# Kernel optimization log

Hardware: AMD Instinct MI355X
Metric: run time of the kernel (lower is better)

The kernel has to match this reference:

```python
import jax, jax.numpy as jnp
import numpy as np
from jax import lax

NUM_TAGS = 19
IN_DIM = 202
HID = 100
B, T = 256, 512


def setup_inputs() -> dict:
    key = jax.random.key(0)
    ks = jax.random.split(key, 16)
    u = lambda k, shape, s: jax.random.uniform(k, shape, jnp.float32, -s, s)
    sh = 1.0 / np.sqrt(HID)
    sl = 1.0 / np.sqrt(2 * HID)
    x = jax.random.normal(ks[0], (B, T, IN_DIM), jnp.float32)
    lengths = jax.random.randint(ks[1], (B,), 1, T + 1)
    raw_tags = jax.random.randint(ks[2], (B, T), 0, NUM_TAGS)
    y = jnp.where(jnp.arange(T)[None, :] < lengths[:, None], raw_tags, -1)
    return dict(
        x=x, y=y,
        w_ih_f=u(ks[3], (HID, IN_DIM), sh), w_hh_f=u(ks[4], (HID, HID), sh),
        b_ih_f=u(ks[5], (HID,), sh), b_hh_f=u(ks[6], (HID,), sh),
        w_ih_b=u(ks[7], (HID, IN_DIM), sh), w_hh_b=u(ks[8], (HID, HID), sh),
        b_ih_b=u(ks[9], (HID,), sh), b_hh_b=u(ks[10], (HID,), sh),
        w_lin=u(ks[11], (NUM_TAGS, 2 * HID), sl), b_lin=u(ks[12], (NUM_TAGS,), sl),
        start_trans=u(ks[13], (NUM_TAGS,), 0.1),
        end_trans=u(ks[14], (NUM_TAGS,), 0.1),
        trans=u(ks[15], (NUM_TAGS, NUM_TAGS), 0.1),
    )


def _rnn_dir(x, w_ih, w_hh, b_ih, b_hh, reverse):
    # torch nn.RNN (tanh) scans over axis 0 of x (batch_first=False semantics)
    def step(h, xt):
        h = jnp.tanh(xt @ w_ih.T + b_ih + h @ w_hh.T + b_hh)
        return h, h
    h0 = jnp.zeros((x.shape[1], w_hh.shape[0]), x.dtype)
    _, hs = lax.scan(step, h0, x, reverse=reverse)
    return hs  # (S, N, HID)


def _emissions(x, w_ih_f, w_hh_f, b_ih_f, b_hh_f, w_ih_b, w_hh_b, b_ih_b, b_hh_b, w_lin, b_lin):
    hf = _rnn_dir(x, w_ih_f, w_hh_f, b_ih_f, b_hh_f, False)
    hb = _rnn_dir(x, w_ih_b, w_hh_b, b_ih_b, b_hh_b, True)
    h = jnp.concatenate([hf, hb], axis=-1)  # (B, T, 200)
    return jax.nn.softmax(h @ w_lin.T + b_lin, axis=2)  # (B, T, 19)


def _crf_llh(em, tags, mask, start, end, trans):
    # emissions (B,T,K) batch_first -> transpose to (T,B,*) for the scans
    em_t = jnp.swapaxes(em, 0, 1)
    tg = jnp.where(jnp.swapaxes(mask, 0, 1), jnp.swapaxes(tags, 0, 1), 0)
    mk = jnp.swapaxes(mask, 0, 1)
    mf = mk.astype(em.dtype)
    # numerator: gold path score
    s0 = start[tg[0]] + jnp.take_along_axis(em_t[0], tg[0][:, None], 1)[:, 0]
    def num_step(carry, inp):
        s, prev = carry
        e, t, m, mb = inp
        emit = jnp.take_along_axis(e, t[:, None], 1)[:, 0]
        s = s + (trans[prev, t] + emit) * m
        prev = jnp.where(mb, t, prev)  # track tag at last valid position
        return (s, prev), None
    (num, last), _ = lax.scan(num_step, (s0, tg[0]), (em_t[1:], tg[1:], mf[1:], mk[1:]))
    num = num + end[last]
    # denominator: masked forward algorithm
    def z_step(s, inp):
        e, mb = inp
        nxt = jax.nn.logsumexp(s[:, :, None] + trans[None] + e[:, None, :], axis=1)
        return jnp.where(mb[:, None], nxt, s), None
    z, _ = lax.scan(z_step, start + em_t[0], (em_t[1:], mk[1:]))
    logz = jax.nn.logsumexp(z + end, axis=1)
    return num - logz  # (B,) log-likelihood per sequence


def _viterbi(em, mask, start, end, trans):
    em_t = jnp.swapaxes(em, 0, 1)
    mk = jnp.swapaxes(mask, 0, 1)
    def fstep(s, inp):
        e, mb = inp
        cand = s[:, :, None] + trans[None] + e[:, None, :]  # (B,K,K)
        nxt = jnp.where(mb[:, None], jnp.max(cand, axis=1), s)
        return nxt, jnp.argmax(cand, axis=1)
    score, hist = lax.scan(fstep, start + em_t[0], (em_t[1:], mk[1:]))  # hist (T-1,B,K)
    best_last = jnp.argmax(score + end, axis=1)  # tag at each sequence end
    def bstep(tag, inp):
        h, mb = inp
        prev = jnp.take_along_axis(h, tag[:, None], 1)[:, 0]
        tag = jnp.where(mb, prev, tag)
        return tag, tag
    _, tags_bt = lax.scan(bstep, best_last, (hist, mk[1:]), reverse=True)  # (T-1,B), position order
    tags = jnp.concatenate([tags_bt, best_last[None]], axis=0)  # (T,B)
    tags = jnp.swapaxes(tags, 0, 1)
    return jnp.where(mask, tags, -1)  # pad with -1 like the torch pad_sequence


def reference(x, y, w_ih_f, w_hh_f, b_ih_f, b_hh_f, w_ih_b, w_hh_b, b_ih_b, b_hh_b, w_lin, b_lin, start_trans, end_trans, trans):
    mask = y != -1
    em = _emissions(x, w_ih_f, w_hh_f, b_ih_f, b_hh_f, w_ih_b, w_hh_b, b_ih_b, b_hh_b, w_lin, b_lin)
    loss = -jnp.sum(_crf_llh(em, y, mask, start_trans, end_trans, trans))  # reduction='sum'
    label = _viterbi(em, mask, start_trans, end_trans, trans)
    return loss, label
```

## Files before the change

kernel.cpp:

```cpp
#include <hip/hip_runtime.h>
#include <hip/hip_bf16.h>

#define B_ 256
#define T_ 512
#define IN_ 202
#define HID_ 100
#define K_ 19

typedef __attribute__((ext_vector_type(8))) short short8v;
typedef __attribute__((ext_vector_type(4))) float f32x4;

__device__ __forceinline__ float rl_f(float v, int l) {
  return __int_as_float(__builtin_amdgcn_readlane(__float_as_int(v), l));
}
__device__ __forceinline__ float bcast_f(float v, int l) {
  return __int_as_float(__builtin_amdgcn_ds_bpermute(l * 4, __float_as_int(v)));
}
__device__ __forceinline__ float fast_tanh(float x) {
  float t = __expf(2.f * x);
  float r = __builtin_amdgcn_rcpf(t + 1.f);
  return fmaf(-2.f, r, 1.f);
}

__global__ __launch_bounds__(256, 1) void k_wprep(
    const float* __restrict__ wf, const float* __restrict__ wb,
    unsigned short* __restrict__ w3) {
  int idx = blockIdx.x * 256 + threadIdx.x;
  if (idx >= 224 * 224) return;
  int c = idx / 224, k = idx - (idx / 224) * 224;
  float v = 0.f;
  if (k < IN_) {
    if (c < 100) v = wf[c * IN_ + k];
    else if (c < 200) v = wb[(c - 100) * IN_ + k];
  }
  unsigned u0 = __float_as_uint(v) & 0xffff0000u;
  float r1 = v - __uint_as_float(u0);
  unsigned u1 = __float_as_uint(r1) & 0xffff0000u;
  float r2 = r1 - __uint_as_float(u1);
  w3[idx] = (unsigned short)(u0 >> 16);
  w3[50176 + idx] = (unsigned short)(u1 >> 16);
  w3[100352 + idx] = (unsigned short)(__float_as_uint(r2) >> 16);
}

__global__ __launch_bounds__(256, 2) void k_ih(
    const float* __restrict__ x, const unsigned short* __restrict__ w3,
    const float* __restrict__ bif, const float* __restrict__ bhf,
    const float* __restrict__ bib, const float* __restrict__ bhb,
    float* __restrict__ pre) {
  __shared__ float xs[128 * 36];
  __shared__ float bsum[224];
  int tid = threadIdx.x;
  int wv = tid >> 6, l = tid & 63;
  long row0 = (long)blockIdx.x * 128;
  for (int u = tid; u < 224; u += 256) {
    float bv = 0.f;
    if (u < 100) bv = bif[u] + bhf[u];
    else if (u < 200) bv = bib[u - 100] + bhb[u - 100];
    bsum[u] = bv;
  }
  int lr = l & 15;
  int kq = l >> 4;
  f32x4 acc[2][14];
#pragma unroll
  for (int m = 0; m < 2; m++)
#pragma unroll
    for (int n = 0; n < 14; n++) acc[m][n] = (f32x4){0.f, 0.f, 0.f, 0.f};
  for (int ck = 0; ck < 7; ck++) {
    int k0 = ck * 32;
    __syncthreads();
#pragma unroll
    for (int i = 0; i < 8; i++) {
      int u = tid + i * 256;
      int r = u >> 4, kp = u & 15;
      int gk = k0 + 2 * kp;
      float2 v = make_float2(0.f, 0.f);
      if (gk < IN_) v = *(const float2*)(x + (row0 + r) * IN_ + gk);
      *(float2*)(&xs[r * 36 + 2 * kp]) = v;
    }
    __syncthreads();
    short8v A0[2], A1[2], A2[2];
#pragma unroll
    for (int m = 0; m < 2; m++) {
      const float* ap = &xs[(wv * 32 + m * 16 + lr) * 36 + kq * 8];
      float4 fa = *(const float4*)(ap);
      float4 fb = *(const float4*)(ap + 4);
      float f[8] = {fa.x, fa.y, fa.z, fa.w, fb.x, fb.y, fb.z, fb.w};
#pragma unroll
      for (int j = 0; j < 8; j++) {
        unsigned u0 = __float_as_uint(f[j]) & 0xffff0000u;
        float r1 = f[j] - __uint_as_float(u0);
        unsigned u1 = __float_as_uint(r1) & 0xffff0000u;
        float r2 = r1 - __uint_as_float(u1);
        A0[m][j] = (short)(u0 >> 16);
        A1[m][j] = (short)(u1 >> 16);
        A2[m][j] = (short)(__float_as_uint(r2) >> 16);
      }
    }
#pragma unroll
    for (int n = 0; n < 14; n++) {
      int col = n * 16 + lr;
      const unsigned short* bp = w3 + (long)col * 224 + k0 + kq * 8;
      short8v B0 = *(const short8v*)(bp);
      short8v B1 = *(const short8v*)(bp + 50176);
      short8v B2 = *(const short8v*)(bp + 100352);
#pragma unroll
      for (int m = 0; m < 2; m++) {
        f32x4 c = acc[m][n];
        c = __builtin_amdgcn_mfma_f32_16x16x32_bf16(A0[m], B0, c, 0, 0, 0);
        c = __builtin_amdgcn_mfma_f32_16x16x32_bf16(A0[m], B1, c, 0, 0, 0);
        c = __builtin_amdgcn_mfma_f32_16x16x32_bf16(A1[m], B0, c, 0, 0, 0);
        c = __builtin_amdgcn_mfma_f32_16x16x32_bf16(A0[m], B2, c, 0, 0, 0);
        c = __builtin_amdgcn_mfma_f32_16x16x32_bf16(A2[m], B0, c, 0, 0, 0);
        c = __builtin_amdgcn_mfma_f32_16x16x32_bf16(A1[m], B1, c, 0, 0, 0);
        c = __builtin_amdgcn_mfma_f32_16x16x32_bf16(A1[m], B2, c, 0, 0, 0);
        c = __builtin_amdgcn_mfma_f32_16x16x32_bf16(A2[m], B1, c, 0, 0, 0);
        acc[m][n] = c;
      }
    }
  }
#pragma unroll
  for (int m = 0; m < 2; m++) {
    long rbase = row0 + wv * 32 + m * 16 + kq * 4;
#pragma unroll
    for (int n = 0; n < 13; n++) {
      int col = n * 16 + lr;
      if (col < 200) {
        float bv = bsum[col];
#pragma unroll
        for (int r = 0; r < 4; r++)
          pre[(rbase + r) * 200 + col] = acc[m][n][r] + bv;
      }
    }
  }
}

template <int KO, int KN, bool OW>
__device__ __forceinline__ void rnn8(
    float* __restrict__ p, long step, int row, bool owns, int qidx,
    const float* __restrict__ w, float (*hb)[104], float (*ps)[104]) {
  float wr[KN];
#pragma unroll
  for (int i = 0; i < KN / 4; i++) {
    float4 w4 = *(const float4*)(w + row * HID_ + KO + 4 * i);
    wr[4 * i + 0] = w4.x; wr[4 * i + 1] = w4.y;
    wr[4 * i + 2] = w4.z; wr[4 * i + 3] = w4.w;
  }
  float a = 0.f;
  if (OW) a = p[row];
  for (int s = 0; s < B_; s++) {
    int cur = s & 1;
    float a_next = 0.f;
    if (OW && s < B_ - 1) a_next = p[step + row];
    float ac0 = OW ? a : 0.f, ac1 = 0.f, ac2 = 0.f, ac3 = 0.f;
#pragma unroll
    for (int i = 0; i < KN / 4; i++) {
      float4 h4 = *(const float4*)(&hb[cur][KO + 4 * i]);
      ac0 = fmaf(h4.x, wr[4 * i + 0], ac0);
      ac1 = fmaf(h4.y, wr[4 * i + 1], ac1);
      ac2 = fmaf(h4.z, wr[4 * i + 2], ac2);
      ac3 = fmaf(h4.w, wr[4 * i + 3], ac3);
    }
    float partial = (ac0 + ac1) + (ac2 + ac3);
    if (!OW && owns) ps[qidx][row] = partial;
    __syncthreads();
    if (OW) {
      float tot = partial + ps[0][row] + ps[1][row] + ps[2][row];
      float hnew = fast_tanh(tot);
      if (owns) {
        p[row] = hnew;
        hb[cur ^ 1][row] = hnew;
      }
    }
    __syncthreads();
    p += step;
    a = a_next;
  }
}

__global__ __launch_bounds__(512, 8) void k_rnn(
    float* __restrict__ pre,
    const float* __restrict__ whf, const float* __restrict__ whb) {
  __shared__ __align__(16) float hb[2][104];
  __shared__ __align__(16) float ps[3][104];
  int bid = blockIdx.x;
  int dir = bid >> 9;
  int t = bid & 511;
  const float* w = dir ? whb : whf;
  int tid = threadIdx.x;
  int wv = tid >> 6, lane = tid & 63;
  int grp = wv & 1;
  int kq = wv >> 1;
  int row = grp ? (64 + (lane < 36 ? lane : 35)) : lane;
  bool owns = grp ? (lane < 36) : true;
  long step = dir ? -(long)(T_ * 200) : (long)(T_ * 200);
  float* p = pre + ((long)(dir ? (B_ - 1) : 0) * T_ + t) * 200 + dir * 100;
  if (tid < 104) hb[0][tid] = 0.f;
  __syncthreads();
  if (kq == 0)      rnn8<0, 16, true >(p, step, row, owns, 0, w, hb, ps);
  else if (kq == 1) rnn8<16, 28, false>(p, step, row, owns, 0, w, hb, ps);
  else if (kq == 2) rnn8<44, 28, false>(p, step, row, owns, 1, w, hb, ps);
  else              rnn8<72, 28, false>(p, step, row, owns, 2, w, hb, ps);
}

__global__ __launch_bounds__(256, 4) void k_lin(
    const float* __restrict__ h, const float* __restrict__ wlin,
    const float* __restrict__ blin, float* __restrict__ em) {
  int tid = threadIdx.x;
  long r0 = ((long)blockIdx.x * 256 + tid) * 2;
  const float* h0 = h + r0 * 200;
  float acc0[K_], acc1[K_];
#pragma unroll
  for (int c = 0; c < K_; c++) { float bb = blin[c]; acc0[c] = bb; acc1[c] = bb; }
  for (int kk = 0; kk < 50; kk++) {
    float4 a = *(const float4*)(h0 + 4 * kk);
    float4 b = *(const float4*)(h0 + 200 + 4 * kk);
#pragma unroll
    for (int c = 0; c < K_; c++) {
      float4 wv = *(const float4*)(wlin + c * 200 + 4 * kk);
      acc0[c] += a.x * wv.x + a.y * wv.y + a.z * wv.z + a.w * wv.w;
      acc1[c] += b.x * wv.x + b.y * wv.y + b.z * wv.z + b.w * wv.w;
    }
  }
  float mx0 = acc0[0], mx1 = acc1[0];
#pragma unroll
  for (int c = 1; c < K_; c++) { mx0 = fmaxf(mx0, acc0[c]); mx1 = fmaxf(mx1, acc1[c]); }
  float s0 = 0.f, s1 = 0.f;
#pragma unroll
  for (int c = 0; c < K_; c++) {
    acc0[c] = __expf(acc0[c] - mx0); s0 += acc0[c];
    acc1[c] = __expf(acc1[c] - mx1); s1 += acc1[c];
  }
  float i0 = 1.f / s0, i1 = 1.f / s1;
  float* e0 = em + r0 * K_;
#pragma unroll
  for (int c = 0; c < K_; c++) { e0[c] = acc0[c] * i0; e0[K_ + c] = acc1[c] * i1; }
}

__global__ __launch_bounds__(128, 1) void k_crf(
    const float* __restrict__ em, const int* __restrict__ y,
    const float* __restrict__ st_g, const float* __restrict__ en_g,
    const float* __restrict__ tr_g,
    float* __restrict__ part, int* __restrict__ cnt,
    float* __restrict__ out) {
  __shared__ __align__(16) float es[T_ * K_];
  __shared__ int ys[T_];
  __shared__ float trs[K_ * K_];
  __shared__ float st[K_], en[K_];
  __shared__ unsigned char hl[511 * K_ + 13];
  int b = blockIdx.x;
  int tid = threadIdx.x;
  int wv = tid >> 6, lane = tid & 63;
  const float4* eb4 = (const float4*)(em + (long)b * T_ * K_);
  for (int u = tid; u < T_ * K_ / 4; u += 128) ((float4*)es)[u] = eb4[u];
  for (int u = tid; u < T_; u += 128) ys[u] = y[b * T_ + u];
  for (int u = tid; u < K_ * K_; u += 128) trs[u] = tr_g[u];
  if (tid < K_) { st[tid] = st_g[tid]; en[tid] = en_g[tid]; }
  __syncthreads();
  int lmin = T_;
  for (int u = lane; u < T_; u += 64)
    if (ys[u] == -1 && u < lmin) lmin = u;
#pragma unroll
  for (int off = 32; off; off >>= 1) {
    int o = __shfl_xor(lmin, off, 64);
    lmin = lmin < o ? lmin : o;
  }
  int len = lmin;

  int jj = lane < K_ ? lane : K_ - 1;
  bool act = lane < K_;
  float enr[20];
#pragma unroll
  for (int q = 0; q < 5; q++) {
    float4 e4 = (q < 4) ? *(const float4*)(&en[4 * q])
                        : make_float4(en[16], en[17], en[18], -1e30f);
    enr[4 * q] = e4.x; enr[4 * q + 1] = e4.y; enr[4 * q + 2] = e4.z; enr[4 * q + 3] = e4.w;
  }

  if (wv == 0) {
    float gacc = 0.f;
    for (int t = 1 + lane; t < len; t += 64)
      gacc += trs[ys[t - 1] * K_ + ys[t]] + es[t * K_ + ys[t]];
#pragma unroll
    for (int off = 32; off; off >>= 1) gacc += __shfl_xor(gacc, off, 64);
    int y0 = ys[0], ylast = ys[len - 1];
    float num = st[y0] + es[y0] + gacc + en[ylast];
    float Ecol[K_];
#pragma unroll
    for (int i = 0; i < K_; i++) Ecol[i] = __expf(trs[i * K_ + jj]);
    float P = __expf(st[jj] + es[jj]);
    int kacc = 0;
    float ee = __expf(es[K_ + jj]);
    for (int t = 1; t < len; t++) {
      float pr[K_];
#pragma unroll
      for (int i = 0; i < K_; i++) pr[i] = bcast_f(P, i);
      int tn = (t + 1 < T_) ? t + 1 : T_ - 1;
      float e_next = es[tn * K_ + jj];
      unsigned pb = __float_as_uint(pr[0]);
      int ex = (int)((pb >> 23) & 0xff);
      float scale = __uint_as_float((unsigned)(254 - ex) << 23);
      kacc += ex - 127;
      float a0 = 0.f, a1 = 0.f, a2 = 0.f, a3 = 0.f;
#pragma unroll
      for (int i = 0; i < K_; i++) {
        if ((i & 3) == 0)      a0 = fmaf(pr[i], Ecol[i], a0);
        else if ((i & 3) == 1) a1 = fmaf(pr[i], Ecol[i], a1);
        else if ((i & 3) == 2) a2 = fmaf(pr[i], Ecol[i], a2);
        else                   a3 = fmaf(pr[i], Ecol[i], a3);
      }
      P = ((((a0 + a1) + (a2 + a3)) * ee)) * scale;
      ee = __expf(e_next);
    }
    {
      float pr[K_];
#pragma unroll
      for (int i = 0; i < K_; i++) pr[i] = bcast_f(P, i);
      float sm = 0.f;
#pragma unroll
      for (int i = 0; i < K_; i++) sm += pr[i] * __expf(enr[i]);
      if (lane == 0) part[b] = __logf(sm) + (float)kacc * 0.6931471805599453f - num;
    }
    int old = -1;
    if (lane == 0) { __threadfence(); old = atomicAdd(cnt, 1); }
    old = __shfl(old, 0, 64);
    if (old == B_ - 1) {
      __threadfence();
      float s = 0.f;
      for (int u = lane; u < B_; u += 64) s += part[u];
#pragma unroll
      for (int off = 32; off; off >>= 1) s += __shfl_xor(s, off, 64);
      if (lane == 0) out[0] = s;
    }
  } else {
    float Tt[K_];
#pragma unroll
    for (int i = 0; i < K_; i++) Tt[i] = trs[i * K_ + jj];
    float V = st[jj] + es[jj];
    float e = es[K_ + jj];
    for (int t = 1; t < len; t++) {
      float vr[K_];
#pragma unroll
      for (int i = 0; i < K_; i++) vr[i] = bcast_f(V, i);
      int tn = (t + 1 < T_) ? t + 1 : T_ - 1;
      float e_next = es[tn * K_ + jj];
      float b0 = -1e30f, b1 = -1e30f, b2 = -1e30f, b3 = -1e30f;
      int a0 = 0, a1 = 5, a2 = 10, a3 = 15;
#pragma unroll
      for (int i = 0; i < 5; i++)  { float c = vr[i] + Tt[i]; if (c > b0) { b0 = c; a0 = i; } }
#pragma unroll
      for (int i = 5; i < 10; i++) { float c = vr[i] + Tt[i]; if (c > b1) { b1 = c; a1 = i; } }
#pragma unroll
      for (int i = 10; i < 15; i++){ float c = vr[i] + Tt[i]; if (c > b2) { b2 = c; a2 = i; } }
#pragma unroll
      for (int i = 15; i < 19; i++){ float c = vr[i] + Tt[i]; if (c > b3) { b3 = c; a3 = i; } }
      if (b1 > b0) { b0 = b1; a0 = a1; }
      if (b2 > b0) { b0 = b2; a0 = a2; }
      if (b3 > b0) { b0 = b3; a0 = a3; }
      if (act) hl[(t - 1) * K_ + lane] = (unsigned char)a0;
      V = b0 + e;
      e = e_next;
    }
    int aa;
    {
      float vr[K_];
#pragma unroll
      for (int i = 0; i < K_; i++) vr[i] = bcast_f(V, i);
      float bb = vr[0] + enr[0]; aa = 0;
#pragma unroll
      for (int i = 1; i < K_; i++) {
        float c = vr[i] + enr[i];
        if (c > bb) { bb = c; aa = i; }
      }
    }
    float* ob = out + 1 + (long)b * T_;
    for (int u = lane; u < T_; u += 64)
      if (u >= len) ob[u] = -1.f;
    int tag = aa;
    if (lane == 0) ob[len - 1] = (float)tag;
    int vc = (act && len >= 2) ? (int)hl[(len - 2) * K_ + lane] : 0;
    for (int ti = len - 2; ti >= 0; ti--) {
      int vn = 0;
      if (ti > 0 && act) vn = (int)hl[(ti - 1) * K_ + lane];
      int ts = __builtin_amdgcn_readfirstlane(tag);
      tag = __builtin_amdgcn_readlane(vc, ts);
      if (lane == 0) ob[ti] = (float)tag;
      vc = vn;
    }
  }
}

extern "C" void kernel_launch(void* const* d_in, const int* in_sizes, int n_in,
                              void* d_out, int out_size, void* d_ws, size_t ws_size,
                              hipStream_t stream) {
  const float* x      = (const float*)d_in[0];
  const int*   y      = (const int*)d_in[1];
  const float* w_ih_f = (const float*)d_in[2];
  const float* w_hh_f = (const float*)d_in[3];
  const float* b_ih_f = (const float*)d_in[4];
  const float* b_hh_f = (const float*)d_in[5];
  const float* w_ih_b = (const float*)d_in[6];
  const float* w_hh_b = (const float*)d_in[7];
  const float* b_ih_b = (const float*)d_in[8];
  const float* b_hh_b = (const float*)d_in[9];
  const float* w_lin  = (const float*)d_in[10];
  const float* b_lin  = (const float*)d_in[11];
  const float* st     = (const float*)d_in[12];
  const float* en     = (const float*)d_in[13];
  const float* trans  = (const float*)d_in[14];

  char* ws = (char*)d_ws;
  const size_t PRE_OFF  = 0;
  const size_t EM_OFF   = 104857600;
  const size_t PART_OFF = EM_OFF + 9961472;
  const size_t CNT_OFF  = PART_OFF + 1024;
  float* PRE  = (float*)(ws + PRE_OFF);
  float* EM   = (float*)(ws + EM_OFF);
  float* PART = (float*)(ws + PART_OFF);
  int*   CNT  = (int*)(ws + CNT_OFF);
  unsigned short* W3 = (unsigned short*)(ws + EM_OFF);
  float* out  = (float*)d_out;

  hipMemsetAsync((void*)CNT, 0, sizeof(int), stream);
  k_wprep<<<196, 256, 0, stream>>>(w_ih_f, w_ih_b, W3);
  k_ih<<<1024, 256, 0, stream>>>(x, W3, b_ih_f, b_hh_f, b_ih_b, b_hh_b, PRE);
  k_rnn<<<1024, 512, 0, stream>>>(PRE, w_hh_f, w_hh_b);
  k_lin<<<256, 256, 0, stream>>>(PRE, w_lin, b_lin, EM);
  k_crf<<<256, 128, 0, stream>>>(EM, y, st, en, trans, PART, CNT, out);
}
```

Baseline: 579.1 us.

## Process two sequences per CRF block to interleave independent recurrences

The CRF kernel now handles two batch rows per block (128 blocks instead of 256), interleaving the forward-algorithm and Viterbi recurrences for both sequences in each time step. This gives each wave two independent dependency chains to hide the latency of the serial per-step bpermute/FMA work, and it uses dynamic LDS sized for two emission tiles and two backpointer buffers. The cost is twice the LDS per block, half as many blocks, and a loop that runs to the longer of the two lengths with per-sequence predication. Label y is also read directly from global memory rather than staged in LDS.

```diff
diff --git a/kernel.cpp b/kernel.cpp
--- a/kernel.cpp
+++ b/kernel.cpp
@@ -6,6 +6,15 @@
 #define IN_ 202
 #define HID_ 100
 #define K_ 19
+
+#define ES0_OFF 0
+#define ES1_OFF 9728
+#define TRS_OFF 19456
+#define STL_OFF 19820
+#define ENL_OFF 19840
+#define HL0_B   79440
+#define HL1_B   89152
+#define CRF2_LDS_B 98880
 
 typedef __attribute__((ext_vector_type(8))) short short8v;
 typedef __attribute__((ext_vector_type(4))) float f32x4;
@@ -242,88 +251,133 @@
     const float* __restrict__ tr_g,
     float* __restrict__ part, int* __restrict__ cnt,
     float* __restrict__ out) {
-  __shared__ __align__(16) float es[T_ * K_];
-  __shared__ int ys[T_];
-  __shared__ float trs[K_ * K_];
-  __shared__ float st[K_], en[K_];
-  __shared__ unsigned char hl[511 * K_ + 13];
-  int b = blockIdx.x;
+  extern __shared__ __align__(16) float S[];
+  unsigned char* hl0 = (unsigned char*)S + HL0_B;
+  unsigned char* hl1 = (unsigned char*)S + HL1_B;
+  int b0 = blockIdx.x, b1 = blockIdx.x + 128;
   int tid = threadIdx.x;
   int wv = tid >> 6, lane = tid & 63;
-  const float4* eb4 = (const float4*)(em + (long)b * T_ * K_);
-  for (int u = tid; u < T_ * K_ / 4; u += 128) ((float4*)es)[u] = eb4[u];
-  for (int u = tid; u < T_; u += 128) ys[u] = y[b * T_ + u];
-  for (int u = tid; u < K_ * K_; u += 128) trs[u] = tr_g[u];
-  if (tid < K_) { st[tid] = st_g[tid]; en[tid] = en_g[tid]; }
+  const float4* eg0 = (const float4*)(em + (long)b0 * T_ * K_);
+  const float4* eg1 = (const float4*)(em + (long)b1 * T_ * K_);
+  for (int u = tid; u < T_ * K_ / 4; u += 128) {
+    ((float4*)(S + ES0_OFF))[u] = eg0[u];
+    ((float4*)(S + ES1_OFF))[u] = eg1[u];
+  }
+  for (int u = tid; u < K_ * K_; u += 128) S[TRS_OFF + u] = tr_g[u];
+  if (tid < K_) { S[STL_OFF + tid] = st_g[tid]; S[ENL_OFF + tid] = en_g[tid]; }
   __syncthreads();
-  int lmin = T_;
-  for (int u = lane; u < T_; u += 64)
-    if (ys[u] == -1 && u < lmin) lmin = u;
+  const float* es0 = S + ES0_OFF;
+  const float* es1 = S + ES1_OFF;
+  const float* trs = S + TRS_OFF;
+  const float* stl = S + STL_OFF;
+  const float* enl = S + ENL_OFF;
+  const int* yb0 = y + (long)b0 * T_;
+  const int* yb1 = y + (long)b1 * T_;
+  int l0 = T_, l1 = T_;
+  for (int u = lane; u < T_; u += 64) {
+    if (yb0[u] == -1 && u < l0) l0 = u;
+    if (yb1[u] == -1 && u < l1) l1 = u;
+  }
 #pragma unroll
   for (int off = 32; off; off >>= 1) {
-    int o = __shfl_xor(lmin, off, 64);
-    lmin = lmin < o ? lmin : o;
-  }
-  int len = lmin;
-
+    int o0 = __shfl_xor(l0, off, 64); l0 = l0 < o0 ? l0 : o0;
+    int o1 = __shfl_xor(l1, off, 64); l1 = l1 < o1 ? l1 : o1;
+  }
+  int len0 = l0, len1 = l1;
+  int lenM = len0 > len1 ? len0 : len1;
   int jj = lane < K_ ? lane : K_ - 1;
   bool act = lane < K_;
-  float enr[20];
-#pragma unroll
-  for (int q = 0; q < 5; q++) {
-    float4 e4 = (q < 4) ? *(const float4*)(&en[4 * q])
-                        : make_float4(en[16], en[17], en[18], -1e30f);
-    enr[4 * q] = e4.x; enr[4 * q + 1] = e4.y; enr[4 * q + 2] = e4.z; enr[4 * q + 3] = e4.w;
-  }
 
   if (wv == 0) {
-    float gacc = 0.f;
-    for (int t = 1 + lane; t < len; t += 64)
-      gacc += trs[ys[t - 1] * K_ + ys[t]] + es[t * K_ + ys[t]];
-#pragma unroll
-    for (int off = 32; off; off >>= 1) gacc += __shfl_xor(gacc, off, 64);
-    int y0 = ys[0], ylast = ys[len - 1];
-    float num = st[y0] + es[y0] + gacc + en[ylast];
+    float g0 = 0.f, g1 = 0.f;
+    for (int t = 1 + lane; t < len0; t += 64)
+      g0 += trs[yb0[t - 1] * K_ + yb0[t]] + es0[t * K_ + yb0[t]];
+    for (int t = 1 + lane; t < len1; t += 64)
+      g1 += trs[yb1[t - 1] * K_ + yb1[t]] + es1[t * K_ + yb1[t]];
+#pragma unroll
+    for (int off = 32; off; off >>= 1) {
+      g0 += __shfl_xor(g0, off, 64);
+      g1 += __shfl_xor(g1, off, 64);
+    }
+    float num0 = stl[yb0[0]] + es0[yb0[0]] + g0 + enl[yb0[len0 - 1]];
+    float num1 = stl[yb1[0]] + es1[yb1[0]] + g1 + enl[yb1[len1 - 1]];
     float Ecol[K_];
 #pragma unroll
     for (int i = 0; i < K_; i++) Ecol[i] = __expf(trs[i * K_ + jj]);
-    float P = __expf(st[jj] + es[jj]);
-    int kacc = 0;
-    float ee = __expf(es[K_ + jj]);
-    for (int t = 1; t < len; t++) {
-      float pr[K_];
-#pragma unroll
-      for (int i = 0; i < K_; i++) pr[i] = bcast_f(P, i);
+    float P0 = __expf(stl[jj] + es0[jj]);
+    float P1 = __expf(stl[jj] + es1[jj]);
+    int kc0 = 0, kc1 = 0;
+    float ee0 = __expf(es0[K_ + jj]);
+    float ee1 = __expf(es1[K_ + jj]);
+    for (int t = 1; t < lenM; t++) {
+      bool q0 = t < len0, q1 = t < len1;
+      float pr0[K_], pr1[K_];
+      if (q0) {
+#pragma unroll
+        for (int i = 0; i < K_; i++) pr0[i] = bcast_f(P0, i);
+      }
+      if (q1) {
+#pragma unroll
+        for (int i = 0; i < K_; i++) pr1[i] = bcast_f(P1, i);
+      }
       int tn = (t + 1 < T_) ? t + 1 : T_ - 1;
-      float e_next = es[tn * K_ + jj];
-      unsigned pb = __float_as_uint(pr[0]);
-      int ex = (int)((pb >> 23) & 0xff);
-      float scale = __uint_as_float((unsigned)(254 - ex) << 23);
-      kacc += ex - 127;
-      float a0 = 0.f, a1 = 0.f, a2 = 0.f, a3 = 0.f;
+      if (q0) {
+        float e_next = es0[tn * K_ + jj];
+        unsigned pb = __float_as_uint(pr0[0]);
+        int ex = (int)((pb >> 23) & 0xff);
+        float scale = __uint_as_float((unsigned)(254 - ex) << 23);
+        kc0 += ex - 127;
+        float a0 = 0.f, a1 = 0.f, a2 = 0.f, a3 = 0.f;
+#pragma unroll
+        for (int i = 0; i < K_; i++) {
+          if ((i & 3) == 0)      a0 = fmaf(pr0[i], Ecol[i], a0);
+          else if ((i & 3) == 1) a1 = fmaf(pr0[i], Ecol[i], a1);
+          else if ((i & 3) == 2) a2 = fmaf(pr0[i], Ecol[i], a2);
+          else                   a3 = fmaf(pr0[i], Ecol[i], a3);
+        }
+        P0 = ((((a0 + a1) + (a2 + a3)) * ee0)) * scale;
+        ee0 = __expf(e_next);
+      }
+      if (q1) {
+        float e_next = es1[tn * K_ + jj];
+        unsigned pb = __float_as_uint(pr1[0]);
+        int ex = (int)((pb >> 23) & 0xff);
+        float scale = __uint_as_float((unsigned)(254 - ex) << 23);
+        kc1 += ex - 127;
+        float a0 = 0.f, a1 = 0.f, a2 = 0.f, a3 = 0.f;
+#pragma unroll
+        for (int i = 0; i < K_; i++) {
+          if ((i & 3) == 0)      a0 = fmaf(pr1[i], Ecol[i], a0);
+          else if ((i & 3) == 1) a1 = fmaf(pr1[i], Ecol[i], a1);
+          else if ((i & 3) == 2) a2 = fmaf(pr1[i], Ecol[i], a2);
+          else                   a3 = fmaf(pr1[i], Ecol[i], a3);
+        }
+        P1 = ((((a0 + a1) + (a2 + a3)) * ee1)) * scale;
+        ee1 = __expf(e_next);
+      }
+    }
+    {
+      float pr0[K_], pr1[K_];
+#pragma unroll
+      for (int i = 0; i < K_; i++) pr0[i] = bcast_f(P0, i);
+#pragma unroll
+      for (int i = 0; i < K_; i++) pr1[i] = bcast_f(P1, i);
+      float s0 = 0.f, s1 = 0.f;
 #pragma unroll
       for (int i = 0; i < K_; i++) {
-        if ((i & 3) == 0)      a0 = fmaf(pr[i], Ecol[i], a0);
-        else if ((i & 3) == 1) a1 = fmaf(pr[i], Ecol[i], a1);
-        else if ((i & 3) == 2) a2 = fmaf(pr[i], Ecol[i], a2);
-        else                   a3 = fmaf(pr[i], Ecol[i], a3);
-      }
-      P = ((((a0 + a1) + (a2 + a3)) * ee)) * scale;
-      ee = __expf(e_next);
-    }
-    {
-      float pr[K_];
-#pragma unroll
-      for (int i = 0; i < K_; i++) pr[i] = bcast_f(P, i);
-      float sm = 0.f;
-#pragma unroll
-      for (int i = 0; i < K_; i++) sm += pr[i] * __expf(enr[i]);
-      if (lane == 0) part[b] = __logf(sm) + (float)kacc * 0.6931471805599453f - num;
+        float ene = __expf(enl[i]);
+        s0 += pr0[i] * ene;
+        s1 += pr1[i] * ene;
+      }
+      if (lane == 0) {
+        part[b0] = __logf(s0) + (float)kc0 * 0.6931471805599453f - num0;
+        part[b1] = __logf(s1) + (float)kc1 * 0.6931471805599453f - num1;
+      }
     }
     int old = -1;
     if (lane == 0) { __threadfence(); old = atomicAdd(cnt, 1); }
     old = __shfl(old, 0, 64);
-    if (old == B_ - 1) {
+    if (old == 127) {
       __threadfence();
       float s = 0.f;
       for (int u = lane; u < B_; u += 64) s += part[u];
@@ -335,56 +389,110 @@
     float Tt[K_];
 #pragma unroll
     for (int i = 0; i < K_; i++) Tt[i] = trs[i * K_ + jj];
-    float V = st[jj] + es[jj];
-    float e = es[K_ + jj];
-    for (int t = 1; t < len; t++) {
-      float vr[K_];
-#pragma unroll
-      for (int i = 0; i < K_; i++) vr[i] = bcast_f(V, i);
+    float V0 = stl[jj] + es0[jj];
+    float V1 = stl[jj] + es1[jj];
+    float e0c = es0[K_ + jj];
+    float e1c = es1[K_ + jj];
+    for (int t = 1; t < lenM; t++) {
+      bool q0 = t < len0, q1 = t < len1;
+      float vr0[K_], vr1[K_];
+      if (q0) {
+#pragma unroll
+        for (int i = 0; i < K_; i++) vr0[i] = bcast_f(V0, i);
+      }
+      if (q1) {
+#pragma unroll
+        for (int i = 0; i < K_; i++) vr1[i] = bcast_f(V1, i);
+      }
       int tn = (t + 1 < T_) ? t + 1 : T_ - 1;
-      float e_next = es[tn * K_ + jj];
-      float b0 = -1e30f, b1 = -1e30f, b2 = -1e30f, b3 = -1e30f;
-      int a0 = 0, a1 = 5, a2 = 10, a3 = 15;
-#pragma unroll
-      for (int i = 0; i < 5; i++)  { float c = vr[i] + Tt[i]; if (c > b0) { b0 = c; a0 = i; } }
-#pragma unroll
-      for (int i = 5; i < 10; i++) { float c = vr[i] + Tt[i]; if (c > b1) { b1 = c; a1 = i; } }
-#pragma unroll
-      for (int i = 10; i < 15; i++){ float c = vr[i] + Tt[i]; if (c > b2) { b2 = c; a2 = i; } }
-#pragma unroll
-      for (int i = 15; i < 19; i++){ float c = vr[i] + Tt[i]; if (c > b3) { b3 = c; a3 = i; } }
-      if (b1 > b0) { b0 = b1; a0 = a1; }
-      if (b2 > b0) { b0 = b2; a0 = a2; }
-      if (b3 > b0) { b0 = b3; a0 = a3; }
-      if (act) hl[(t - 1) * K_ + lane] = (unsigned char)a0;
-      V = b0 + e;
-      e = e_next;
-    }
-    int aa;
+      if (q0) {
+        float e_next = es0[tn * K_ + jj];
+        float c0 = -1e30f, c1 = -1e30f, c2 = -1e30f, c3 = -1e30f;
+        int a0 = 0, a1 = 5, a2 = 10, a3 = 15;
+#pragma unroll
+        for (int i = 0; i < 5; i++)  { float c = vr0[i] + Tt[i]; if (c > c0) { c0 = c; a0 = i; } }
+#pragma unroll
+        for (int i = 5; i < 10; i++) { float c = vr0[i] + Tt[i]; if (c > c1) { c1 = c; a1 = i; } }
+#pragma unroll
+        for (int i = 10; i < 15; i++){ float c = vr0[i] + Tt[i]; if (c > c2) { c2 = c; a2 = i; } }
+#pragma unroll
+        for (int i = 15; i < 19; i++){ float c = vr0[i] + Tt[i]; if (c > c3) { c3 = c; a3 = i; } }
+        if (c1 > c0) { c0 = c1; a0 = a1; }
+        if (c2 > c0) { c0 = c2; a0 = a2; }
+        if (c3 > c0) { c0 = c3; a0 = a3; }
+        if (act) hl0[(t - 1) * K_ + lane] = (unsigned char)a0;
+        V0 = c0 + e0c;
+        e0c = e_next;
+      }
+      if (q1) {
+        float e_next = es1[tn * K_ + jj];
+        float c0 = -1e30f, c1 = -1e30f, c2 = -1e30f, c3 = -1e30f;
+        int a0 = 0, a1 = 5, a2 = 10, a3 = 15;
+#pragma unroll
+        for (int i = 0; i < 5; i++)  { float c = vr1[i] + Tt[i]; if (c > c0) { c0 = c; a0 = i; } }
+#pragma unroll
+        for (int i = 5; i < 10; i++) { float c = vr1[i] + Tt[i]; if (c > c1) { c1 = c; a1 = i; } }
+#pragma unroll
+        for (int i = 10; i < 15; i++){ float c = vr1[i] + Tt[i]; if (c > c2) { c2 = c; a2 = i; } }
+#pragma unroll
+        for (int i = 15; i < 19; i++){ float c = vr1[i] + Tt[i]; if (c > c3) { c3 = c; a3 = i; } }
+        if (c1 > c0) { c0 = c1; a0 = a1; }
+        if (c2 > c0) { c0 = c2; a0 = a2; }
+        if (c3 > c0) { c0 = c3; a0 = a3; }
+        if (act) hl1[(t - 1) * K_ + lane] = (unsigned char)a0;
+        V1 = c0 + e1c;
+        e1c = e_next;
+      }
+    }
     {
       float vr[K_];
 #pragma unroll
-      for (int i = 0; i < K_; i++) vr[i] = bcast_f(V, i);
-      float bb = vr[0] + enr[0]; aa = 0;
+      for (int i = 0; i < K_; i++) vr[i] = bcast_f(V0, i);
+      float bb = vr[0] + enl[0]; int aa = 0;
 #pragma unroll
       for (int i = 1; i < K_; i++) {
-        float c = vr[i] + enr[i];
+        float c = vr[i] + enl[i];
         if (c > bb) { bb = c; aa = i; }
       }
-    }
-    float* ob = out + 1 + (long)b * T_;
-    for (int u = lane; u < T_; u += 64)
-      if (u >= len) ob[u] = -1.f;
-    int tag = aa;
-    if (lane == 0) ob[len - 1] = (float)tag;
-    int vc = (act && len >= 2) ? (int)hl[(len - 2) * K_ + lane] : 0;
-    for (int ti = len - 2; ti >= 0; ti--) {
-      int vn = 0;
-      if (ti > 0 && act) vn = (int)hl[(ti - 1) * K_ + lane];
-      int ts = __builtin_amdgcn_readfirstlane(tag);
-      tag = __builtin_amdgcn_readlane(vc, ts);
-      if (lane == 0) ob[ti] = (float)tag;
-      vc = vn;
+      float* ob = out + 1 + (long)b0 * T_;
+      for (int u = lane; u < T_; u += 64)
+        if (u >= len0) ob[u] = -1.f;
+      int tag = aa;
+      if (lane == 0) ob[len0 - 1] = (float)tag;
+      int vc = (act && len0 >= 2) ? (int)hl0[(len0 - 2) * K_ + lane] : 0;
+      for (int ti = len0 - 2; ti >= 0; ti--) {
+        int vn = 0;
+        if (ti > 0 && act) vn = (int)hl0[(ti - 1) * K_ + lane];
+        int ts = __builtin_amdgcn_readfirstlane(tag);
+        tag = __builtin_amdgcn_readlane(vc, ts);
+        if (lane == 0) ob[ti] = (float)tag;
+        vc = vn;
+      }
+    }
+    {
+      float vr[K_];
+#pragma unroll
+      for (int i = 0; i < K_; i++) vr[i] = bcast_f(V1, i);
+      float bb = vr[0] + enl[0]; int aa = 0;
+#pragma unroll
+      for (int i = 1; i < K_; i++) {
+        float c = vr[i] + enl[i];
+        if (c > bb) { bb = c; aa = i; }
+      }
+      float* ob = out + 1 + (long)b1 * T_;
+      for (int u = lane; u < T_; u += 64)
+        if (u >= len1) ob[u] = -1.f;
+      int tag = aa;
+      if (lane == 0) ob[len1 - 1] = (float)tag;
+      int vc = (act && len1 >= 2) ? (int)hl1[(len1 - 2) * K_ + lane] : 0;
+      for (int ti = len1 - 2; ti >= 0; ti--) {
+        int vn = 0;
+        if (ti > 0 && act) vn = (int)hl1[(ti - 1) * K_ + lane];
+        int ts = __builtin_amdgcn_readfirstlane(tag);
+        tag = __builtin_amdgcn_readlane(vc, ts);
+        if (lane == 0) ob[ti] = (float)tag;
+        vc = vn;
+      }
     }
   }
 }
@@ -420,10 +528,12 @@
   unsigned short* W3 = (unsigned short*)(ws + EM_OFF);
   float* out  = (float*)d_out;
 
+  hipFuncSetAttribute((const void*)k_crf,
+                      hipFuncAttributeMaxDynamicSharedMemorySize, CRF2_LDS_B);
   hipMemsetAsync((void*)CNT, 0, sizeof(int), stream);
   k_wprep<<<196, 256, 0, stream>>>(w_ih_f, w_ih_b, W3);
   k_ih<<<1024, 256, 0, stream>>>(x, W3, b_ih_f, b_hh_f, b_ih_b, b_hh_b, PRE);
   k_rnn<<<1024, 512, 0, stream>>>(PRE, w_hh_f, w_hh_b);
   k_lin<<<256, 256, 0, stream>>>(PRE, w_lin, b_lin, EM);
-  k_crf<<<256, 128, 0, stream>>>(EM, y, st, en, trans, PART, CNT, out);
-}
+  k_crf<<<128, 128, CRF2_LDS_B, stream>>>(EM, y, st, en, trans, PART, CNT, out);
+}
```

Measured after the change: 785.9 us. +35.7%, slower.
